# Kernel tuning notes

Measured on AMD Instinct MI355X. Metric: run time of the kernel, lower is better.

The kernel has to match this reference:

```python
import jax, jax.numpy as jnp
import numpy as np

DECAY = 0.99
EPS = 1e-05


def setup_inputs() -> dict:
    key = jax.random.key(0)
    k1, k2 = jax.random.split(key)
    B, D, T, K = 8, 256, 2048, 8192
    x = jax.random.normal(k1, (B, D, T), dtype=jnp.float32)
    # xavier_uniform init for the [K, D] codebook
    bound = float(np.sqrt(6.0 / (K + D)))
    embeddings = jax.random.uniform(k2, (K, D), dtype=jnp.float32,
                                    minval=-bound, maxval=bound)
    return {"x": x, "embeddings": embeddings}


def reference(x, embeddings):
    # x: [B, D, T]; embeddings: [K, D]. Training-mode forward (EMA update, STE).
    B, D, T = x.shape
    K = embeddings.shape[0]

    vq_in = jnp.transpose(x, (0, 2, 1))          # [B, T, D]
    flatten = vq_in.reshape(-1, D)               # [N, D], N = B*T

    # get_code_indices: squared-L2 distances via expansion + argmin
    distances = (jnp.sum(flatten ** 2, axis=1, keepdims=True)
                 + jnp.sum(embeddings ** 2, axis=1)
                 - 2.0 * flatten @ embeddings.T)  # [N, K]
    encoding_indices = jnp.argmin(distances, axis=1)  # [N]

    # quantize: codebook gather (uses pre-update embeddings, as in torch)
    vq_out = embeddings[encoding_indices].reshape(vq_in.shape)  # [B, T, D]

    # --- EMA codebook update (no_grad block; first step: counter=1, hidden=0) ---
    # one-hot column sums == bincount; one-hot^T @ flatten == segment_sum
    cluster_size = jax.ops.segment_sum(
        jnp.ones_like(encoding_indices, dtype=flatten.dtype),
        encoding_indices, num_segments=K)                       # [K]
    dw = jax.ops.segment_sum(flatten, encoding_indices, num_segments=K)  # [K, D]

    one_m_decay = 1.0 - DECAY
    bias_corr = 1.0 - DECAY ** 1  # counter == 1
    ema_cs = (cluster_size * one_m_decay) / bias_corr           # == cluster_size
    ema_dw = (dw * one_m_decay) / bias_corr                     # == dw

    n = jnp.sum(ema_cs)
    ema_cs = (ema_cs + EPS) / (n + K * EPS) * n
    new_embeddings = ema_dw / ema_cs[:, None]                   # [K, D]

    # straight-through estimator
    vq_out_st = vq_in + jax.lax.stop_gradient(vq_out - vq_in)   # [B, T, D]

    quantized = jnp.transpose(vq_out_st, (0, 2, 1))             # [B, D, T]
    vq_in_bdt = jnp.transpose(vq_in, (0, 2, 1))                 # [B, D, T]
    return (quantized, vq_in_bdt, jax.lax.stop_gradient(quantized),
            new_embeddings)
```

## Files before the change

kernel.cpp:

```cpp
#include <hip/hip_runtime.h>
#include <stdint.h>

#define B_ 8
#define D_ 256
#define T_ 2048
#define K_ 8192
#define N_ (B_*T_)

typedef __attribute__((ext_vector_type(8))) __bf16 bf16x8;
typedef __attribute__((ext_vector_type(4))) __bf16 bf16x4;
typedef __attribute__((ext_vector_type(2))) __bf16 bf16x2;
typedef __attribute__((ext_vector_type(4))) float f32x4;


__global__ __launch_bounds__(256) void prep_e_kernel(const float* __restrict__ E,
                                                     __bf16* __restrict__ E3,
                                                     float* __restrict__ sse) {
    int row  = blockIdx.x * 4 + (threadIdx.x >> 6);
    int lane = threadIdx.x & 63;
    int d    = lane * 4;
    float4 v = *(const float4*)(E + (size_t)row * D_ + d);
    __bf16 h0 = (__bf16)v.x, h1 = (__bf16)v.y, h2 = (__bf16)v.z, h3 = (__bf16)v.w;
    __bf16 l0 = (__bf16)(v.x - (float)h0), l1 = (__bf16)(v.y - (float)h1);
    __bf16 l2 = (__bf16)(v.z - (float)h2), l3 = (__bf16)(v.w - (float)h3);
    bf16x4 hv = {h0, h1, h2, h3};
    bf16x4 lv = {l0, l1, l2, l3};
    int kh  = d >> 5;
    int s   = (d >> 3) & 3;
    int pos = d & 7;
    *(bf16x4*)(E3 + ((size_t)((kh    ) * 4 + s) * K_ + row) * 8 + pos) = lv;
    *(bf16x4*)(E3 + ((size_t)((8 + kh) * 4 + s) * K_ + row) * 8 + pos) = hv;
    float sq = __fadd_rn(__fadd_rn(__fmul_rn(v.x, v.x), __fmul_rn(v.y, v.y)),
                         __fadd_rn(__fmul_rn(v.z, v.z), __fmul_rn(v.w, v.w)));
    #pragma unroll
    for (int off = 32; off > 0; off >>= 1) sq += __shfl_down(sq, off);
    if (lane == 0) sse[row] = sq;
}

__global__ __launch_bounds__(256) void prep_x_kernel(const float* __restrict__ x,
                                                     __bf16* __restrict__ X3,
                                                     float* __restrict__ ssx) {
    __shared__ float tile[64][65];
    __shared__ float part[64][4];
    int bidx = blockIdx.x;
    int b    = bidx >> 7;
    int dblk = (bidx >> 5) & 3;
    int tblk = bidx & 31;
    int d0 = dblk * 64, t0 = tblk * 64;
    const float* xp = x + (size_t)b * D_ * T_;
    {
        int tl = threadIdx.x & 63, th = threadIdx.x >> 6;
        float s = 0.f;
        #pragma unroll
        for (int i = 0; i < 16; i++) {
            int d = i * 4 + th;
            float v = xp[(size_t)(d0 + d) * T_ + t0 + tl];
            tile[d][tl] = v;
            s = __fadd_rn(s, __fmul_rn(v, v));
        }
        part[tl][th] = s;
    }
    __syncthreads();
    if (threadIdx.x < 64) {
        float tot = __fadd_rn(__fadd_rn(__fadd_rn(part[threadIdx.x][0],
                    part[threadIdx.x][1]), part[threadIdx.x][2]), part[threadIdx.x][3]);
        atomicAdd(ssx + b * T_ + t0 + threadIdx.x, tot);
    }
    {
        int t  = threadIdx.x & 63;
        int g0 = threadIdx.x >> 6;
        size_t n = (size_t)b * T_ + t0 + t;
        #pragma unroll
        for (int i = 0; i < 2; i++) {
            int dg = g0 + i * 4;
            int p  = (d0 >> 3) + dg;
            bf16x8 hv, lv;
            #pragma unroll
            for (int e = 0; e < 8; e++) {
                float v = tile[dg * 8 + e][t];
                __bf16 h = (__bf16)v;
                hv[e] = h;
                lv[e] = (__bf16)(v - (float)h);
            }
            *(bf16x8*)(X3 + ((size_t)(p     ) * N_ + n) * 8) = hv;
            *(bf16x8*)(X3 + ((size_t)(p + 32) * N_ + n) * 8) = lv;
        }
    }
}


#define GLD16(g, l) __builtin_amdgcn_global_load_lds(                           \
    (const __attribute__((address_space(1))) void*)(g),                         \
    (__attribute__((address_space(3))) void*)(l), 16, 0, 0)

#define VMW(n) do { asm volatile("s_waitcnt vmcnt(" #n ")" ::: "memory");       \
                    __builtin_amdgcn_sched_barrier(0); } while (0)
#define BAR() do { asm volatile("" ::: "memory");                               \
                   __builtin_amdgcn_s_barrier();                                \
                   asm volatile("" ::: "memory");                               \
                   __builtin_amdgcn_sched_barrier(0); } while (0)

__device__ __forceinline__ void stage_tile(const __bf16* __restrict__ E3,
                                           const __bf16* __restrict__ X3,
                                           __bf16* smem, int t, int buf,
                                           int c0, int r0, int tid) {
    const int phA = ((t >= 8) ? 8 : 0) + (t & 7);
    const int phB = ((t >= 8 && t < 16) ? 8 : 0) + (t & 7);
    __bf16* lA = smem + buf * 8192 + ((tid >> 6) << 9);
    const __bf16* gA = E3 + ((size_t)(phA * 4) * K_ + c0 + tid) * 8;
    #pragma unroll
    for (int o = 0; o < 4; o++)
        GLD16(gA + (size_t)o * K_ * 8, lA + o * 2048);
    __bf16* lB = smem + 24576 + buf * 4096 + ((tid >> 6) << 9);
    #pragma unroll
    for (int o = 0; o < 2; o++) {
        const __bf16* gB = X3 + ((size_t)(phB * 4 + 2 * o + (tid >> 7)) * N_
                                 + r0 + (tid & 127)) * 8;
        GLD16(gB, lB + o * 2048);
    }
}

__device__ __forceinline__ void compute_tile(const __bf16* smem, int buf,
                                             f32x4 acc[8][4],
                                             int wm, int wn, int l) {
    const __bf16* pa = smem + buf * 8192 + (l >> 4) * 2048
                       + (wm * 128 + (l & 15)) * 8;
    const __bf16* pb = smem + 24576 + buf * 4096 + (l >> 4) * 1024
                       + (wn * 64 + (l & 15)) * 8;
    bf16x8 af[8], bf[4];
    #pragma unroll
    for (int i = 0; i < 8; i++) af[i] = *(const bf16x8*)(pa + i * 128);
    #pragma unroll
    for (int j = 0; j < 4; j++) bf[j] = *(const bf16x8*)(pb + j * 128);
    __builtin_amdgcn_s_setprio(1);
    #pragma unroll
    for (int i = 0; i < 8; i++)
        #pragma unroll
        for (int j = 0; j < 4; j++)
            acc[i][j] = __builtin_amdgcn_mfma_f32_16x16x32_bf16(
                af[i], bf[j], acc[i][j], 0, 0, 0);
    __builtin_amdgcn_s_setprio(0);
}

__global__ __launch_bounds__(256, 2) void dist_kernel(
    const __bf16* __restrict__ E3, const __bf16* __restrict__ X3,
    const float* __restrict__ ssx, const float* __restrict__ sse,
    unsigned long long* __restrict__ best)
{
    __shared__ __bf16 smem[36864];

    const int tid = threadIdx.x;
    const int l   = tid & 63;
    const int w   = tid >> 6;
    const int wm  = w >> 1;
    const int wn  = w & 1;

    const int bid = blockIdx.x;
    const int xq  = bid & 7;
    const int i_  = bid >> 3;
    const int c0  = (xq * 4 + (i_ & 3)) * 256;
    const int r0  = (i_ >> 2) * 128;

    f32x4 acc[8][4];
    #pragma unroll
    for (int i = 0; i < 8; i++)
        #pragma unroll
        for (int j = 0; j < 4; j++) acc[i][j] = (f32x4)0.f;

    stage_tile(E3, X3, smem, 0, 0, c0, r0, tid);
    stage_tile(E3, X3, smem, 1, 1, c0, r0, tid);
    VMW(6);
    BAR();

    #pragma unroll 1
    for (int it = 0; it < 8; it++) {
        const int t = 3 * it;
        stage_tile(E3, X3, smem, t + 2, 2, c0, r0, tid);
        compute_tile(smem, 0, acc, wm, wn, l);
        VMW(6);
        BAR();
        if (it < 7) stage_tile(E3, X3, smem, t + 3, 0, c0, r0, tid);
        compute_tile(smem, 1, acc, wm, wn, l);
        if (it < 7) { VMW(6); } else { VMW(0); }
        BAR();
        if (it < 7) stage_tile(E3, X3, smem, t + 4, 1, c0, r0, tid);
        compute_tile(smem, 2, acc, wm, wn, l);
        if (it < 7) { VMW(6); BAR(); }
    }

    #pragma unroll
    for (int j = 0; j < 4; j++) {
        int xrow = r0 + wn * 64 + j * 16 + (l & 15);
        float sx = ssx[xrow];
        unsigned long long m = ~0ull;
        #pragma unroll
        for (int i = 0; i < 8; i++) {
            int cbase = c0 + wm * 128 + i * 16 + (l >> 4) * 4;
            float4 sc = *(const float4*)(sse + cbase);
            f32x4 a = acc[i][j];
            float d0 = (sx + sc.x) - 2.0f * a[0];
            float d1 = (sx + sc.y) - 2.0f * a[1];
            float d2 = (sx + sc.z) - 2.0f * a[2];
            float d3 = (sx + sc.w) - 2.0f * a[3];
            unsigned long long p;
            p = ((unsigned long long)__float_as_uint(d0) << 32) | (unsigned)(cbase + 0);
            if (p < m) m = p;
            p = ((unsigned long long)__float_as_uint(d1) << 32) | (unsigned)(cbase + 1);
            if (p < m) m = p;
            p = ((unsigned long long)__float_as_uint(d2) << 32) | (unsigned)(cbase + 2);
            if (p < m) m = p;
            p = ((unsigned long long)__float_as_uint(d3) << 32) | (unsigned)(cbase + 3);
            if (p < m) m = p;
        }
        unsigned long long o;
        o = __shfl_xor(m, 16); if (o < m) m = o;
        o = __shfl_xor(m, 32); if (o < m) m = o;
        if ((l >> 4) == 0) atomicMin(best + xrow, m);
    }
}

__global__ __launch_bounds__(256) void scatter_kernel(
    const float* __restrict__ x, const float* __restrict__ E,
    const unsigned long long* __restrict__ best,
    float* __restrict__ out, int* __restrict__ cs, float* __restrict__ dw)
{
    __shared__ float tx[64][68];
    __shared__ float te[64][68];
    __shared__ int sidx[64];

    const int blk = blockIdx.x;
    const int b   = blk >> 5;
    const int t0  = (blk & 31) * 64;
    const int tid = threadIdx.x;
    const int n0  = b * T_ + t0;

    if (tid < 64) {
        int ix = (int)(best[n0 + tid] & 0xffffffffu);
        sidx[tid] = ix;
        atomicAdd(cs + ix, 1);
    }
    __syncthreads();

    const int t4   = (tid & 15) * 4;
    const int dg   = tid >> 4;
    const int l    = tid & 63;
    const int w    = tid >> 6;
    const int nsub = l >> 4;
    const int dl4  = (l & 15) * 4;

    float* o0 = out;
    float* o1 = out + (size_t)N_ * D_;
    float* o2 = out + 2 * (size_t)N_ * D_;

    for (int dc = 0; dc < 4; dc++) {
        const int d0 = dc * 64;
        #pragma unroll
        for (int r = 0; r < 4; r++) {
            int d = r * 16 + dg;
            size_t gi = ((size_t)(b * D_ + d0 + d)) * T_ + t0 + t4;
            float4 v = *(const float4*)(x + gi);
            *(float4*)&tx[d][t4] = v;
            *(float4*)(o1 + gi) = v;
        }
        #pragma unroll
        for (int i = 0; i < 4; i++) {
            int nl  = w * 16 + i * 4 + nsub;
            int row = sidx[nl];
            float4 ev = *(const float4*)(E + (size_t)row * D_ + d0 + dl4);
            te[dl4 + 0][nl] = ev.x;
            te[dl4 + 1][nl] = ev.y;
            te[dl4 + 2][nl] = ev.z;
            te[dl4 + 3][nl] = ev.w;
        }
        __syncthreads();
        #pragma unroll
        for (int r = 0; r < 4; r++) {
            int d = r * 16 + dg;
            float4 v = *(const float4*)&te[d][t4];
            size_t gi = ((size_t)(b * D_ + d0 + d)) * T_ + t0 + t4;
            *(float4*)(o0 + gi) = v;
            *(float4*)(o2 + gi) = v;
        }
        #pragma unroll
        for (int i = 0; i < 16; i++) {
            int nl = w * 16 + i;
            atomicAdd(dw + (size_t)sidx[nl] * D_ + d0 + l, tx[l][nl]);
        }
        __syncthreads();
    }
}

__global__ __launch_bounds__(256) void finalize_kernel(
    const int* __restrict__ cs, const float* __restrict__ dw,
    float* __restrict__ out3)
{
    int k = blockIdx.x;
    int d = threadIdx.x;
    const float C = 0.00999999977648258209228515625f;
    float c   = (float)cs[k];
    float ecs = (c * C) / C;
    float edw = (dw[(size_t)k * D_ + d] * C) / C;
    float n = 16384.0f;
    float denom = (ecs + 1e-5f) / (n + (float)K_ * 1e-5f) * n;
    out3[(size_t)k * D_ + d] = edw / denom;
}

extern "C" void kernel_launch(void* const* d_in, const int* in_sizes, int n_in,
                              void* d_out, int out_size, void* d_ws, size_t ws_size,
                              hipStream_t stream) {
    const float* x = (const float*)d_in[0];
    const float* E = (const float*)d_in[1];
    float* out = (float*)d_out;

    char* ws = (char*)d_ws;
    unsigned long long* best = (unsigned long long*)(ws);
    int*   cs  = (int*)  (ws + 131072);
    float* dw  = (float*)(ws + 163840);
    float* sse = (float*)(ws + 8552448);
    float* ssx = (float*)(ws + 8585216);

    __bf16* X3 = (__bf16*)out;
    __bf16* E3 = (__bf16*)(out + 2 * (size_t)N_ * D_);

    hipMemsetAsync(best, 0xFF, (size_t)N_ * 8, stream);
    hipMemsetAsync(cs, 0, 8650752 - 131072, stream);

    prep_e_kernel<<<K_ / 4, 256, 0, stream>>>(E, E3, sse);
    prep_x_kernel<<<1024, 256, 0, stream>>>(x, X3, ssx);
    dist_kernel<<<4096, 256, 0, stream>>>(E3, X3, ssx, sse, best);
    scatter_kernel<<<256, 256, 0, stream>>>(x, E, best, out, cs, dw);
    finalize_kernel<<<K_, 256, 0, stream>>>(cs, dw, out + 3 * (size_t)N_ * D_);
}
```

Measured before the change: 230.2 us.

## Reuse E-hi fragments across both X planes and switch to double buffering

The split-bf16 GEMM previously ran 24 phases, each loading an E slice and an X slice. Phases E_lo·X_hi, E_hi·X_hi and E_hi·X_lo are now regrouped into 16 phases, where the E-hi phases load both X planes and reuse the A fragments for two MFMA batches. This cuts LDS traffic and global loads of E. The pipeline drops from a triple buffer with partial vmcnt waits to a double buffer with a full vmcnt(0) wait every iteration, which may expose more load latency. Shared memory use falls slightly.

```diff
diff --git a/kernel.cpp b/kernel.cpp
--- a/kernel.cpp
+++ b/kernel.cpp
@@ -93,45 +93,49 @@
     (const __attribute__((address_space(1))) void*)(g),                         \
     (__attribute__((address_space(3))) void*)(l), 16, 0, 0)
 
-#define VMW(n) do { asm volatile("s_waitcnt vmcnt(" #n ")" ::: "memory");       \
+#define VMW0() do { asm volatile("s_waitcnt vmcnt(0)" ::: "memory");            \
                     __builtin_amdgcn_sched_barrier(0); } while (0)
 #define BAR() do { asm volatile("" ::: "memory");                               \
                    __builtin_amdgcn_s_barrier();                                \
                    asm volatile("" ::: "memory");                               \
                    __builtin_amdgcn_sched_barrier(0); } while (0)
 
-__device__ __forceinline__ void stage_tile(const __bf16* __restrict__ E3,
-                                           const __bf16* __restrict__ X3,
-                                           __bf16* smem, int t, int buf,
-                                           int c0, int r0, int tid) {
-    const int phA = ((t >= 8) ? 8 : 0) + (t & 7);
-    const int phB = ((t >= 8 && t < 16) ? 8 : 0) + (t & 7);
-    __bf16* lA = smem + buf * 8192 + ((tid >> 6) << 9);
-    const __bf16* gA = E3 + ((size_t)(phA * 4) * K_ + c0 + tid) * 8;
+__device__ __forceinline__ void stage_any(const __bf16* __restrict__ E3,
+                                          const __bf16* __restrict__ X3,
+                                          __bf16* smem, int p, int buf,
+                                          int c0, int r0, int tid) {
+    const int kh = p & 7;
+    __bf16* slot = smem + buf * 16384;
+    __bf16* lA = slot + ((tid >> 6) << 9);
+    const __bf16* gA = E3 + ((size_t)(p * 4) * K_ + c0 + tid) * 8;
     #pragma unroll
     for (int o = 0; o < 4; o++)
         GLD16(gA + (size_t)o * K_ * 8, lA + o * 2048);
-    __bf16* lB = smem + 24576 + buf * 4096 + ((tid >> 6) << 9);
-    #pragma unroll
-    for (int o = 0; o < 2; o++) {
-        const __bf16* gB = X3 + ((size_t)(phB * 4 + 2 * o + (tid >> 7)) * N_
-                                 + r0 + (tid & 127)) * 8;
-        GLD16(gB, lB + o * 2048);
-    }
-}
-
-__device__ __forceinline__ void compute_tile(const __bf16* smem, int buf,
-                                             f32x4 acc[8][4],
-                                             int wm, int wn, int l) {
-    const __bf16* pa = smem + buf * 8192 + (l >> 4) * 2048
-                       + (wm * 128 + (l & 15)) * 8;
-    const __bf16* pb = smem + 24576 + buf * 4096 + (l >> 4) * 1024
-                       + (wn * 64 + (l & 15)) * 8;
-    bf16x8 af[8], bf[4];
-    #pragma unroll
-    for (int i = 0; i < 8; i++) af[i] = *(const bf16x8*)(pa + i * 128);
-    #pragma unroll
-    for (int j = 0; j < 4; j++) bf[j] = *(const bf16x8*)(pb + j * 128);
+    if (p < 8) {
+        __bf16* lB0 = slot + 8192 + ((tid >> 6) << 9);
+        #pragma unroll
+        for (int o = 0; o < 2; o++) {
+            const __bf16* gB = X3 + ((size_t)(kh * 4 + 2 * o + (tid >> 7)) * N_
+                                     + r0 + (tid & 127)) * 8;
+            GLD16(gB, lB0 + o * 2048);
+        }
+    } else {
+        __bf16* lB0 = slot + 8192 + ((tid >> 6) << 9);
+        __bf16* lB1 = slot + 12288 + ((tid >> 6) << 9);
+        #pragma unroll
+        for (int o = 0; o < 2; o++) {
+            const __bf16* gB0 = X3 + ((size_t)(32 + kh * 4 + 2 * o + (tid >> 7)) * N_
+                                      + r0 + (tid & 127)) * 8;
+            GLD16(gB0, lB0 + o * 2048);
+            const __bf16* gB1 = X3 + ((size_t)(kh * 4 + 2 * o + (tid >> 7)) * N_
+                                      + r0 + (tid & 127)) * 8;
+            GLD16(gB1, lB1 + o * 2048);
+        }
+    }
+}
+
+__device__ __forceinline__ void mfma32(f32x4 acc[8][4], const bf16x8 (&af)[8],
+                                       const bf16x8 (&bf)[4]) {
     __builtin_amdgcn_s_setprio(1);
     #pragma unroll
     for (int i = 0; i < 8; i++)
@@ -147,7 +151,7 @@
     const float* __restrict__ ssx, const float* __restrict__ sse,
     unsigned long long* __restrict__ best)
 {
-    __shared__ __bf16 smem[36864];
+    __shared__ __bf16 smem[32768];
 
     const int tid = threadIdx.x;
     const int l   = tid & 63;
@@ -167,25 +171,33 @@
         #pragma unroll
         for (int j = 0; j < 4; j++) acc[i][j] = (f32x4)0.f;
 
-    stage_tile(E3, X3, smem, 0, 0, c0, r0, tid);
-    stage_tile(E3, X3, smem, 1, 1, c0, r0, tid);
-    VMW(6);
+    stage_any(E3, X3, smem, 0, 0, c0, r0, tid);
+    VMW0();
     BAR();
 
     #pragma unroll 1
-    for (int it = 0; it < 8; it++) {
-        const int t = 3 * it;
-        stage_tile(E3, X3, smem, t + 2, 2, c0, r0, tid);
-        compute_tile(smem, 0, acc, wm, wn, l);
-        VMW(6);
+    for (int t = 0; t < 16; t++) {
+        const int buf = t & 1;
+        if (t < 15) stage_any(E3, X3, smem, t + 1, buf ^ 1, c0, r0, tid);
+        const __bf16* slot = smem + buf * 16384;
+        const __bf16* pa = slot + (l >> 4) * 2048 + (wm * 128 + (l & 15)) * 8;
+        const __bf16* pb0 = slot + 8192 + (l >> 4) * 1024 + (wn * 64 + (l & 15)) * 8;
+        bf16x8 af[8], bf[4];
+        #pragma unroll
+        for (int i = 0; i < 8; i++) af[i] = *(const bf16x8*)(pa + i * 128);
+        #pragma unroll
+        for (int j = 0; j < 4; j++) bf[j] = *(const bf16x8*)(pb0 + j * 128);
+        mfma32(acc, af, bf);
+        if (t >= 8) {
+            const __bf16* pb1 = slot + 12288 + (l >> 4) * 1024
+                                + (wn * 64 + (l & 15)) * 8;
+            bf16x8 bg[4];
+            #pragma unroll
+            for (int j = 0; j < 4; j++) bg[j] = *(const bf16x8*)(pb1 + j * 128);
+            mfma32(acc, af, bg);
+        }
+        VMW0();
         BAR();
-        if (it < 7) stage_tile(E3, X3, smem, t + 3, 0, c0, r0, tid);
-        compute_tile(smem, 1, acc, wm, wn, l);
-        if (it < 7) { VMW(6); } else { VMW(0); }
-        BAR();
-        if (it < 7) stage_tile(E3, X3, smem, t + 4, 1, c0, r0, tid);
-        compute_tile(smem, 2, acc, wm, wn, l);
-        if (it < 7) { VMW(6); BAR(); }
     }
 
     #pragma unroll
```

Measured after the change: 222.9 us (median of 2 runs). 3.1% less time.

## Reuse staged X-hi tile across E-hi and E-lo passes in split-bf16 GEMM

Applied to the files above, without the earlier changes.

Restructures the three-pass split-bf16 distance GEMM (Eh*Xh, Eh*Xl, El*Xh) so that each X-hi tile is staged once into shared memory and kept resident for both the E-hi and E-lo products, instead of being reloaded per pass. The K loop becomes 8 half-steps, each with two sub-stages, and uses separate double buffers for X-hi and X-lo plus a triple-buffered A ring. Shared memory moves to 80KB of dynamic allocation, which may lower occupancy below the two blocks per CU requested by the launch bounds. It also adds more register pressure from holding X-hi fragments across a barrier.

```diff
diff --git a/kernel.cpp b/kernel.cpp
--- a/kernel.cpp
+++ b/kernel.cpp
@@ -100,38 +100,30 @@
                    asm volatile("" ::: "memory");                               \
                    __builtin_amdgcn_sched_barrier(0); } while (0)
 
-__device__ __forceinline__ void stage_tile(const __bf16* __restrict__ E3,
-                                           const __bf16* __restrict__ X3,
-                                           __bf16* smem, int t, int buf,
-                                           int c0, int r0, int tid) {
-    const int phA = ((t >= 8) ? 8 : 0) + (t & 7);
-    const int phB = ((t >= 8 && t < 16) ? 8 : 0) + (t & 7);
-    __bf16* lA = smem + buf * 8192 + ((tid >> 6) << 9);
-    const __bf16* gA = E3 + ((size_t)(phA * 4) * K_ + c0 + tid) * 8;
+__device__ __forceinline__ void stage_A(const __bf16* __restrict__ E3,
+                                        __bf16* slot, int panel,
+                                        int c0, int tid) {
+    __bf16* lA = slot + ((tid >> 6) << 9);
+    const __bf16* gA = E3 + ((size_t)(panel * 4) * K_ + c0 + tid) * 8;
     #pragma unroll
     for (int o = 0; o < 4; o++)
         GLD16(gA + (size_t)o * K_ * 8, lA + o * 2048);
-    __bf16* lB = smem + 24576 + buf * 4096 + ((tid >> 6) << 9);
+}
+
+__device__ __forceinline__ void stage_B(const __bf16* __restrict__ X3,
+                                        __bf16* slot, int panelBase,
+                                        int r0, int tid) {
+    __bf16* lB = slot + ((tid >> 6) << 9);
     #pragma unroll
     for (int o = 0; o < 2; o++) {
-        const __bf16* gB = X3 + ((size_t)(phB * 4 + 2 * o + (tid >> 7)) * N_
+        const __bf16* gB = X3 + ((size_t)(panelBase + 2 * o + (tid >> 7)) * N_
                                  + r0 + (tid & 127)) * 8;
         GLD16(gB, lB + o * 2048);
     }
 }
 
-__device__ __forceinline__ void compute_tile(const __bf16* smem, int buf,
-                                             f32x4 acc[8][4],
-                                             int wm, int wn, int l) {
-    const __bf16* pa = smem + buf * 8192 + (l >> 4) * 2048
-                       + (wm * 128 + (l & 15)) * 8;
-    const __bf16* pb = smem + 24576 + buf * 4096 + (l >> 4) * 1024
-                       + (wn * 64 + (l & 15)) * 8;
-    bf16x8 af[8], bf[4];
-    #pragma unroll
-    for (int i = 0; i < 8; i++) af[i] = *(const bf16x8*)(pa + i * 128);
-    #pragma unroll
-    for (int j = 0; j < 4; j++) bf[j] = *(const bf16x8*)(pb + j * 128);
+__device__ __forceinline__ void mfma32(f32x4 acc[8][4], const bf16x8 (&af)[8],
+                                       const bf16x8 (&bf)[4]) {
     __builtin_amdgcn_s_setprio(1);
     #pragma unroll
     for (int i = 0; i < 8; i++)
@@ -147,7 +139,7 @@
     const float* __restrict__ ssx, const float* __restrict__ sse,
     unsigned long long* __restrict__ best)
 {
-    __shared__ __bf16 smem[36864];
+    extern __shared__ __bf16 smem[];
 
     const int tid = threadIdx.x;
     const int l   = tid & 63;
@@ -167,25 +159,58 @@
         #pragma unroll
         for (int j = 0; j < 4; j++) acc[i][j] = (f32x4)0.f;
 
-    stage_tile(E3, X3, smem, 0, 0, c0, r0, tid);
-    stage_tile(E3, X3, smem, 1, 1, c0, r0, tid);
+    __bf16* smA0 = smem;
+    __bf16* smXh = smem + 24576;
+    __bf16* smXl = smem + 32768;
+
+    const int aoff  = (l >> 4) * 2048 + (wm * 128 + (l & 15)) * 8;
+    const int boff  = (l >> 4) * 1024 + (wn * 64 + (l & 15)) * 8;
+
+    stage_A(E3, smA0 + 0 * 8192, 0, c0, tid);
+    stage_B(X3, smXh + 0 * 4096, 0, r0, tid);
+    stage_A(E3, smA0 + 1 * 8192, 8, c0, tid);
+    stage_B(X3, smXl + 0 * 4096, 32, r0, tid);
     VMW(6);
     BAR();
 
-    #pragma unroll 1
-    for (int it = 0; it < 8; it++) {
-        const int t = 3 * it;
-        stage_tile(E3, X3, smem, t + 2, 2, c0, r0, tid);
-        compute_tile(smem, 0, acc, wm, wn, l);
-        VMW(6);
+    #pragma unroll
+    for (int kh = 0; kh < 8; kh++) {
+        const int aE = (2 * kh) % 3;
+        const int aH = (2 * kh + 1) % 3;
+        const int xs = kh & 1;
+        bf16x8 af[8], bxh[4], bxl[4];
+
+        if (kh < 7) {
+            stage_A(E3, smA0 + ((2 * kh + 2) % 3) * 8192, kh + 1, c0, tid);
+            stage_B(X3, smXh + (xs ^ 1) * 4096, (kh + 1) * 4, r0, tid);
+        }
+        {
+            const __bf16* pa = smA0 + aE * 8192 + aoff;
+            const __bf16* pb = smXh + xs * 4096 + boff;
+            #pragma unroll
+            for (int i = 0; i < 8; i++) af[i] = *(const bf16x8*)(pa + i * 128);
+            #pragma unroll
+            for (int j = 0; j < 4; j++) bxh[j] = *(const bf16x8*)(pb + j * 128);
+        }
+        mfma32(acc, af, bxh);
+        if (kh < 7) { VMW(6); } else { VMW(0); }
         BAR();
-        if (it < 7) stage_tile(E3, X3, smem, t + 3, 0, c0, r0, tid);
-        compute_tile(smem, 1, acc, wm, wn, l);
-        if (it < 7) { VMW(6); } else { VMW(0); }
-        BAR();
-        if (it < 7) stage_tile(E3, X3, smem, t + 4, 1, c0, r0, tid);
-        compute_tile(smem, 2, acc, wm, wn, l);
-        if (it < 7) { VMW(6); BAR(); }
+
+        if (kh < 7) {
+            stage_A(E3, smA0 + ((2 * kh + 3) % 3) * 8192, 8 + kh + 1, c0, tid);
+            stage_B(X3, smXl + (xs ^ 1) * 4096, 32 + (kh + 1) * 4, r0, tid);
+        }
+        {
+            const __bf16* pa = smA0 + aH * 8192 + aoff;
+            const __bf16* pb = smXl + xs * 4096 + boff;
+            #pragma unroll
+            for (int i = 0; i < 8; i++) af[i] = *(const bf16x8*)(pa + i * 128);
+            #pragma unroll
+            for (int j = 0; j < 4; j++) bxl[j] = *(const bf16x8*)(pb + j * 128);
+        }
+        mfma32(acc, af, bxl);
+        mfma32(acc, af, bxh);
+        if (kh < 7) { VMW(6); BAR(); }
     }
 
     #pragma unroll
@@ -325,9 +350,12 @@
     hipMemsetAsync(best, 0xFF, (size_t)N_ * 8, stream);
     hipMemsetAsync(cs, 0, 8650752 - 131072, stream);
 
+    hipFuncSetAttribute((const void*)dist_kernel,
+                        hipFuncAttributeMaxDynamicSharedMemorySize, 81920);
+
     prep_e_kernel<<<K_ / 4, 256, 0, stream>>>(E, E3, sse);
     prep_x_kernel<<<1024, 256, 0, stream>>>(x, X3, ssx);
-    dist_kernel<<<4096, 256, 0, stream>>>(E3, X3, ssx, sse, best);
+    dist_kernel<<<4096, 256, 81920, stream>>>(E3, X3, ssx, sse, best);
     scatter_kernel<<<256, 256, 0, stream>>>(x, E, best, out, cs, dw);
     finalize_kernel<<<K_, 256, 0, stream>>>(cs, dw, out + 3 * (size_t)N_ * D_);
 }
```

After: 205.3 us. 1.12x faster.
